# Optimization experiments

Measured on AMD Instinct MI355X. Metric: run time of the kernel, lower is better.

## Reference

```python
import jax, jax.numpy as jnp
import numpy as np

N_NODES = 100000
N_EDGES = 1600000
IN_F = 128
OUT_F = 128
EDGE_F = 16


def setup_inputs() -> dict:
    key = jax.random.key(0)
    ks = jax.random.split(key, 8)
    H = jax.random.normal(ks[0], (N_NODES, IN_F), dtype=jnp.float32)
    edge_index = jax.random.randint(ks[1], (2, N_EDGES), 0, N_ODES_ := N_NODES, dtype=jnp.int64) if False else jax.random.randint(ks[1], (2, N_EDGES), 0, N_NODES, dtype=jnp.int32).astype(jnp.int64)
    edge_attr = jax.random.normal(ks[2], (N_EDGES, EDGE_F), dtype=jnp.float32)
    We = jax.random.normal(ks[3], (EDGE_F, IN_F), dtype=jnp.float32) * (1.0 / np.sqrt(EDGE_F))
    be = jnp.zeros((IN_F,), dtype=jnp.float32)
    W1 = jax.random.normal(ks[4], (IN_F, OUT_F), dtype=jnp.float32) * (1.0 / np.sqrt(IN_F))
    b1 = jnp.zeros((OUT_F,), dtype=jnp.float32)
    W2 = jax.random.normal(ks[5], (OUT_F, OUT_F), dtype=jnp.float32) * (1.0 / np.sqrt(OUT_F))
    b2 = jnp.zeros((OUT_F,), dtype=jnp.float32)
    return {"H": H, "edge_index": edge_index, "edge_attr": edge_attr,
            "We": We, "be": be, "W1": W1, "b1": b1, "W2": W2, "b2": b2}


def reference(H, edge_index, edge_attr, We, be, W1, b1, W2, b2):
    # edge_mlp: Linear(edge_attr_dim -> in_features)
    edge_messages = edge_attr @ We + be                       # [E, in_f]
    # gather by src, add edge messages
    messages = H[edge_index[0]] + edge_messages               # [E, in_f]
    # scatter_add by dst with dim_size = N
    aggregated = jax.ops.segment_sum(messages, edge_index[1], num_segments=H.shape[0])  # [N, in_f]
    # node_mlp: Linear -> ReLU -> Linear
    h = jax.nn.relu(aggregated @ W1 + b1)                     # [N, out_f]
    out = h @ W2 + b2                                         # [N, out_f]
    return out
```

## Files before the change

kernel.cpp:

```cpp
#include <hip/hip_runtime.h>

#define IN_F 128
#define EF 16

typedef short bf16x8 __attribute__((ext_vector_type(8)));
typedef float f32x4  __attribute__((ext_vector_type(4)));

__device__ __forceinline__ unsigned short f2b(float f) {
    unsigned b = __float_as_uint(f);
    b += 0x7fffu + ((b >> 16) & 1u);
    return (unsigned short)(b >> 16);
}
__device__ __forceinline__ float blo(unsigned u) { return __uint_as_float(u << 16); }
__device__ __forceinline__ float bhi(unsigned u) { return __uint_as_float(u & 0xffff0000u); }


__global__ __launch_bounds__(256) void pre_kernel(
    const float* __restrict__ H, unsigned short* __restrict__ Hb, int n4,
    const int* __restrict__ ei, int* __restrict__ counts,
    int* __restrict__ rank, int E,
    const float* __restrict__ W1, unsigned short* __restrict__ W1t,
    const float* __restrict__ W2, unsigned short* __restrict__ W2t,
    int h2b_blocks, int hist_blocks)
{
    int b = blockIdx.x;
    if (b < h2b_blocks) {
        int i = b * 256 + threadIdx.x;
        if (i < n4) {
            float4 v = ((const float4*)H)[i];
            ushort4 r;
            r.x = f2b(v.x); r.y = f2b(v.y); r.z = f2b(v.z); r.w = f2b(v.w);
            ((ushort4*)Hb)[i] = r;
        }
    } else if (b < h2b_blocks + hist_blocks) {
        int e = (b - h2b_blocks) * 256 + threadIdx.x;
        if (e < E) rank[e] = atomicAdd(&counts[ei[E + e]], 1);
    } else {
        int idx = (b - h2b_blocks - hist_blocks) * 256 + threadIdx.x;
        int w = idx >> 14;
        int r = idx & 16383;
        int n = r >> 7, k = r & 127;
        if (w == 0) W1t[n * IN_F + k] = f2b(W1[k * IN_F + n]);
        else        W2t[n * IN_F + k] = f2b(W2[k * IN_F + n]);
    }
}

__global__ __launch_bounds__(256) void hist_kernel(
    const int* __restrict__ ei, int* __restrict__ counts,
    int* __restrict__ rank, int E)
{
    int e = blockIdx.x * 256 + threadIdx.x;
    if (e >= E) return;
    rank[e] = atomicAdd(&counts[ei[E + e]], 1);
}

__global__ __launch_bounds__(256) void scan_blocks_kernel(
    const int* __restrict__ in, int* __restrict__ out,
    int* __restrict__ partials, int n)
{
    __shared__ int sdata[256];
    const int t = threadIdx.x;
    const int idx0 = blockIdx.x * 1024 + t * 4;
    int v[4];
    #pragma unroll
    for (int i = 0; i < 4; i++) { int idx = idx0 + i; v[i] = (idx < n) ? in[idx] : 0; }
    int s = v[0] + v[1] + v[2] + v[3];
    sdata[t] = s;
    __syncthreads();
    for (int off = 1; off < 256; off <<= 1) {
        int x = (t >= off) ? sdata[t - off] : 0;
        __syncthreads();
        sdata[t] += x;
        __syncthreads();
    }
    if (t == 255) partials[blockIdx.x] = sdata[255];
    int run = (t > 0) ? sdata[t - 1] : 0;
    #pragma unroll
    for (int i = 0; i < 4; i++) {
        int idx = idx0 + i;
        if (idx < n) out[idx] = run;
        run += v[i];
    }
}

__global__ __launch_bounds__(256) void scan_add_fused_kernel(
    int* __restrict__ out, const int* __restrict__ partials, int n)
{
    __shared__ int sw[4];
    const int t = threadIdx.x;
    const int g = blockIdx.x >> 2;
    int v = 0;
    for (int j = t; j < g; j += 256) v += partials[j];
    #pragma unroll
    for (int off = 1; off < 64; off <<= 1) v += __shfl_xor(v, off, 64);
    if ((t & 63) == 0) sw[t >> 6] = v;
    __syncthreads();
    int P = sw[0] + sw[1] + sw[2] + sw[3];
    int idx = blockIdx.x * 256 + t;
    if (idx < n) out[idx] += P;
}

__global__ __launch_bounds__(256) void build_kernel(
    const int* __restrict__ ei, int2* __restrict__ sorted,
    const int* __restrict__ offsets, const int* __restrict__ rank, int E)
{
    int e = blockIdx.x * 256 + threadIdx.x;
    if (e >= E) return;
    int src = ei[e];
    int dst = ei[E + e];
    int pos = offsets[dst] + rank[e];
    sorted[pos] = make_int2(src, e);
}

__global__ __launch_bounds__(256) void ea_reduce_kernel(
    const float* __restrict__ EA,
    const int2* __restrict__ sorted,
    const int* __restrict__ offsets,
    float* __restrict__ aggE,
    int N)
{
    int n = blockIdx.x * 4 + (threadIdx.x >> 6);
    if (n >= N) return;
    int lane = threadIdx.x & 63;
    int sub  = lane >> 4;
    int f    = lane & 15;
    int s = offsets[n];
    int e_end = offsets[n + 1];
    float acc = 0.f;
    int i = s + sub;
    for (; i + 4 < e_end; i += 8) {
        int e0 = sorted[i].y;
        int e1 = sorted[i + 4].y;
        float v0 = EA[(long long)e0 * EF + f];
        float v1 = EA[(long long)e1 * EF + f];
        acc += v0 + v1;
    }
    for (; i < e_end; i += 4) {
        int e0 = sorted[i].y;
        acc += EA[(long long)e0 * EF + f];
    }
    acc += __shfl_xor(acc, 16, 64);
    acc += __shfl_xor(acc, 32, 64);
    if (sub == 0) aggE[n * EF + f] = acc;
}

__global__ __launch_bounds__(256) void gather_agg_kernel(
    const unsigned short* __restrict__ Hb,
    const int2* __restrict__ sorted,
    const int* __restrict__ offsets,
    const float* __restrict__ aggE,
    const float* __restrict__ We,
    const float* __restrict__ be,
    unsigned short* __restrict__ Ab,
    int N)
{
    int n = blockIdx.x * 4 + (threadIdx.x >> 6);
    if (n >= N) return;
    int lane = threadIdx.x & 63;
    int half = lane >> 5;
    int l32  = lane & 31;
    int s = offsets[n];
    int e_end = offsets[n + 1];
    float a0 = 0.f, a1 = 0.f, a2 = 0.f, a3 = 0.f;
    int i = s + half;
    for (; i + 6 < e_end; i += 8) {
        int s0 = sorted[i].x;
        int s1 = sorted[i + 2].x;
        int s2 = sorted[i + 4].x;
        int s3 = sorted[i + 6].x;
        uint2 u0 = *(const uint2*)(Hb + (long long)s0 * IN_F + l32 * 4);
        uint2 u1 = *(const uint2*)(Hb + (long long)s1 * IN_F + l32 * 4);
        uint2 u2 = *(const uint2*)(Hb + (long long)s2 * IN_F + l32 * 4);
        uint2 u3 = *(const uint2*)(Hb + (long long)s3 * IN_F + l32 * 4);
        a0 += (blo(u0.x) + blo(u1.x)) + (blo(u2.x) + blo(u3.x));
        a1 += (bhi(u0.x) + bhi(u1.x)) + (bhi(u2.x) + bhi(u3.x));
        a2 += (blo(u0.y) + blo(u1.y)) + (blo(u2.y) + blo(u3.y));
        a3 += (bhi(u0.y) + bhi(u1.y)) + (bhi(u2.y) + bhi(u3.y));
    }
    for (; i < e_end; i += 2) {
        int se = sorted[i].x;
        uint2 u = *(const uint2*)(Hb + (long long)se * IN_F + l32 * 4);
        a0 += blo(u.x); a1 += bhi(u.x); a2 += blo(u.y); a3 += bhi(u.y);
    }
    a0 += __shfl_xor(a0, 32, 64);
    a1 += __shfl_xor(a1, 32, 64);
    a2 += __shfl_xor(a2, 32, 64);
    a3 += __shfl_xor(a3, 32, 64);

    const int c4 = l32 * 4;
    const float deg = (float)(e_end - s);
    float4 bev = *(const float4*)&be[c4];
    float vx = a0 + deg * bev.x;
    float vy = a1 + deg * bev.y;
    float vz = a2 + deg * bev.z;
    float vw = a3 + deg * bev.w;
    #pragma unroll
    for (int k = 0; k < EF; k++) {
        float ak = aggE[n * EF + k];
        float4 w = *(const float4*)&We[k * IN_F + c4];
        vx += ak * w.x; vy += ak * w.y; vz += ak * w.z; vw += ak * w.w;
    }
    if (half == 0) {
        ushort4 o;
        o.x = f2b(vx); o.y = f2b(vy); o.z = f2b(vz); o.w = f2b(vw);
        *(ushort4*)&Ab[(long long)n * IN_F + c4] = o;
    }
}

__global__ __launch_bounds__(256) void gather_f32_kernel(
    const float* __restrict__ H,
    const float* __restrict__ EA,
    const int2* __restrict__ sorted,
    const int* __restrict__ offsets,
    float* __restrict__ agg,
    float* __restrict__ aggE,
    float* __restrict__ degf,
    int N)
{
    int n = blockIdx.x * 4 + (threadIdx.x >> 6);
    if (n >= N) return;
    int lane = threadIdx.x & 63;
    int half = lane >> 5;
    int l32  = lane & 31;
    int s = offsets[n];
    int e_end = offsets[n + 1];
    float4 acc = make_float4(0.f, 0.f, 0.f, 0.f);
    float accE = 0.f;
    int i = s + half;
    for (; i + 6 < e_end; i += 8) {
        int2 s0 = sorted[i];
        int2 s1 = sorted[i + 2];
        int2 s2 = sorted[i + 4];
        int2 s3 = sorted[i + 6];
        float4 v0 = *(const float4*)(H + (long long)s0.x * IN_F + l32 * 4);
        float4 v1 = *(const float4*)(H + (long long)s1.x * IN_F + l32 * 4);
        float4 v2 = *(const float4*)(H + (long long)s2.x * IN_F + l32 * 4);
        float4 v3 = *(const float4*)(H + (long long)s3.x * IN_F + l32 * 4);
        float e0 = 0.f, e1 = 0.f, e2 = 0.f, e3 = 0.f;
        if (l32 < EF) {
            e0 = EA[(long long)s0.y * EF + l32];
            e1 = EA[(long long)s1.y * EF + l32];
            e2 = EA[(long long)s2.y * EF + l32];
            e3 = EA[(long long)s3.y * EF + l32];
        }
        acc.x += (v0.x + v1.x) + (v2.x + v3.x);
        acc.y += (v0.y + v1.y) + (v2.y + v3.y);
        acc.z += (v0.z + v1.z) + (v2.z + v3.z);
        acc.w += (v0.w + v1.w) + (v2.w + v3.w);
        accE  += (e0 + e1) + (e2 + e3);
    }
    for (; i < e_end; i += 2) {
        int2 se = sorted[i];
        float4 v = *(const float4*)(H + (long long)se.x * IN_F + l32 * 4);
        acc.x += v.x; acc.y += v.y; acc.z += v.z; acc.w += v.w;
        if (l32 < EF) accE += EA[(long long)se.y * EF + l32];
    }
    acc.x += __shfl_xor(acc.x, 32, 64);
    acc.y += __shfl_xor(acc.y, 32, 64);
    acc.z += __shfl_xor(acc.z, 32, 64);
    acc.w += __shfl_xor(acc.w, 32, 64);
    accE  += __shfl_xor(accE, 32, 64);
    if (half == 0) {
        *(float4*)(agg + (long long)n * IN_F + l32 * 4) = acc;
        if (l32 < EF) aggE[n * EF + l32] = accE;
        if (l32 == 0) degf[n] = (float)(e_end - s);
    }
}

__global__ __launch_bounds__(256) void edge_scatter_kernel(
    const float* __restrict__ H,
    const int* __restrict__ ei,
    const float* __restrict__ EA,
    float* __restrict__ agg,
    float* __restrict__ aggE,
    float* __restrict__ deg,
    int E)
{
    long long gid = (long long)blockIdx.x * 256 + threadIdx.x;
    int e = (int)(gid >> 7);
    if (e >= E) return;
    int f = (int)(gid & 127);
    int src = ei[e];
    int dst = ei[E + e];
    float m = H[(long long)src * IN_F + f];
    atomicAdd(&agg[(long long)dst * IN_F + f], m);
    if (f < EF) atomicAdd(&aggE[dst * EF + f], EA[e * EF + f]);
    if (f == 0) atomicAdd(&deg[dst], 1.0f);
}


#define XPITCH 136
__global__ __launch_bounds__(256) void mlp_mfma_kernel(
    const unsigned short* __restrict__ Ab,
    const unsigned short* __restrict__ W1t,
    const unsigned short* __restrict__ W2t,
    const float* __restrict__ b1, const float* __restrict__ b2,
    float* __restrict__ out, int N)
{
    __shared__ unsigned short sW[128 * XPITCH];
    __shared__ unsigned short sX[64 * XPITCH];
    const int t    = threadIdx.x;
    const int tile = blockIdx.x * 64;
    const int lane = t & 63;
    const int wv   = t >> 6;
    const int quad = lane >> 4;
    const int lr   = lane & 15;
    const int M0   = wv * 16;

    {
        const uint4 z = make_uint4(0, 0, 0, 0);
        #pragma unroll
        for (int j = 0; j < 4; j++) {
            int idx = t + 256 * j;
            int row = idx >> 4, c = idx & 15;
            uint4 v = z;
            if (tile + row < N) v = ((const uint4*)Ab)[(long long)(tile + row) * 16 + c];
            ((uint4*)sX)[row * 17 + c] = v;
        }
        #pragma unroll
        for (int j = 0; j < 8; j++) {
            int idx = t + 256 * j;
            int row = idx >> 4, c = idx & 15;
            ((uint4*)sW)[row * 17 + c] = ((const uint4*)W1t)[idx];
        }
    }
    __syncthreads();

    f32x4 acc[8];
    bf16x8 af[4];
    const f32x4 zero = {0.f, 0.f, 0.f, 0.f};

    #pragma unroll
    for (int kt = 0; kt < 4; kt++)
        af[kt] = *(const bf16x8*)&sX[(M0 + lr) * XPITCH + kt * 32 + quad * 8];
    #pragma unroll
    for (int nt = 0; nt < 8; nt++) {
        acc[nt] = zero;
        #pragma unroll
        for (int kt = 0; kt < 4; kt++) {
            bf16x8 bf = *(const bf16x8*)&sW[(nt * 16 + lr) * XPITCH + kt * 32 + quad * 8];
            acc[nt] = __builtin_amdgcn_mfma_f32_16x16x32_bf16(af[kt], bf, acc[nt], 0, 0, 0);
        }
    }
    #pragma unroll
    for (int nt = 0; nt < 8; nt++) {
        int col = nt * 16 + lr;
        float bias = b1[col];
        #pragma unroll
        for (int r = 0; r < 4; r++) {
            float v = fmaxf(acc[nt][r] + bias, 0.f);
            sX[(M0 + quad * 4 + r) * XPITCH + col] = f2b(v);
        }
    }
    __syncthreads();
    #pragma unroll
    for (int j = 0; j < 8; j++) {
        int idx = t + 256 * j;
        int row = idx >> 4, c = idx & 15;
        ((uint4*)sW)[row * 17 + c] = ((const uint4*)W2t)[idx];
    }
    __syncthreads();

    #pragma unroll
    for (int kt = 0; kt < 4; kt++)
        af[kt] = *(const bf16x8*)&sX[(M0 + lr) * XPITCH + kt * 32 + quad * 8];
    #pragma unroll
    for (int nt = 0; nt < 8; nt++) {
        acc[nt] = zero;
        #pragma unroll
        for (int kt = 0; kt < 4; kt++) {
            bf16x8 bf = *(const bf16x8*)&sW[(nt * 16 + lr) * XPITCH + kt * 32 + quad * 8];
            acc[nt] = __builtin_amdgcn_mfma_f32_16x16x32_bf16(af[kt], bf, acc[nt], 0, 0, 0);
        }
    }
    #pragma unroll
    for (int nt = 0; nt < 8; nt++) {
        int col = nt * 16 + lr;
        float bias = b2[col];
        #pragma unroll
        for (int r = 0; r < 4; r++) {
            int row = tile + M0 + quad * 4 + r;
            if (row < N) out[(long long)row * IN_F + col] = acc[nt][r] + bias;
        }
    }
}

__global__ __launch_bounds__(256) void node_mlp_kernel(
    float* agg_out,
    const float* __restrict__ aggE,
    const float* __restrict__ degf,
    const float* __restrict__ We, const float* __restrict__ be,
    const float* __restrict__ W1, const float* __restrict__ b1,
    const float* __restrict__ W2, const float* __restrict__ b2,
    int N)
{
    __shared__ float sA[32][IN_F];
    __shared__ float sH[32][IN_F];
    const int t  = threadIdx.x;
    const int c4 = (t & 31) * 4;
    const int r0 = t >> 5;

    const int tile = blockIdx.x * 32;
    if (tile >= N) return;
    int rows = N - tile;
    if (rows > 32) rows = 32;

    {
        const float4 bev = *(const float4*)&be[c4];
        #pragma unroll
        for (int i = 0; i < 4; i++) {
            int rr = r0 + 8 * i;
            float4 v = make_float4(0.f, 0.f, 0.f, 0.f);
            if (rr < rows) {
                long long r = tile + rr;
                v = *(const float4*)&agg_out[r * IN_F + c4];
                float d = degf[r];
                v.x += d * bev.x; v.y += d * bev.y; v.z += d * bev.z; v.w += d * bev.w;
                #pragma unroll
                for (int k = 0; k < EF; k++) {
                    float a = aggE[r * EF + k];
                    float4 w = *(const float4*)&We[k * IN_F + c4];
                    v.x += a * w.x; v.y += a * w.y; v.z += a * w.z; v.w += a * w.w;
                }
            }
            *(float4*)&sA[rr][c4] = v;
        }
    }
    __syncthreads();
    {
        const float4 bv = *(const float4*)&b1[c4];
        float4 a0 = bv, a1 = bv, a2 = bv, a3 = bv;
        for (int k = 0; k < IN_F; k++) {
            float4 w = *(const float4*)&W1[k * IN_F + c4];
            float x0 = sA[r0][k], x1 = sA[r0 + 8][k], x2 = sA[r0 + 16][k], x3 = sA[r0 + 24][k];
            a0.x += x0 * w.x; a0.y += x0 * w.y; a0.z += x0 * w.z; a0.w += x0 * w.w;
            a1.x += x1 * w.x; a1.y += x1 * w.y; a1.z += x1 * w.z; a1.w += x1 * w.w;
            a2.x += x2 * w.x; a2.y += x2 * w.y; a2.z += x2 * w.z; a2.w += x2 * w.w;
            a3.x += x3 * w.x; a3.y += x3 * w.y; a3.z += x3 * w.z; a3.w += x3 * w.w;
        }
        a0.x = fmaxf(a0.x, 0.f); a0.y = fmaxf(a0.y, 0.f); a0.z = fmaxf(a0.z, 0.f); a0.w = fmaxf(a0.w, 0.f);
        a1.x = fmaxf(a1.x, 0.f); a1.y = fmaxf(a1.y, 0.f); a1.z = fmaxf(a1.z, 0.f); a1.w = fmaxf(a1.w, 0.f);
        a2.x = fmaxf(a2.x, 0.f); a2.y = fmaxf(a2.y, 0.f); a2.z = fmaxf(a2.z, 0.f); a2.w = fmaxf(a2.w, 0.f);
        a3.x = fmaxf(a3.x, 0.f); a3.y = fmaxf(a3.y, 0.f); a3.z = fmaxf(a3.z, 0.f); a3.w = fmaxf(a3.w, 0.f);
        *(float4*)&sH[r0][c4]      = a0;
        *(float4*)&sH[r0 + 8][c4]  = a1;
        *(float4*)&sH[r0 + 16][c4] = a2;
        *(float4*)&sH[r0 + 24][c4] = a3;
    }
    __syncthreads();
    {
        const float4 bv = *(const float4*)&b2[c4];
        float4 a0 = bv, a1 = bv, a2 = bv, a3 = bv;
        for (int k = 0; k < IN_F; k++) {
            float4 w = *(const float4*)&W2[k * IN_F + c4];
            float x0 = sH[r0][k], x1 = sH[r0 + 8][k], x2 = sH[r0 + 16][k], x3 = sH[r0 + 24][k];
            a0.x += x0 * w.x; a0.y += x0 * w.y; a0.z += x0 * w.z; a0.w += x0 * w.w;
            a1.x += x1 * w.x; a1.y += x1 * w.y; a1.z += x1 * w.z; a1.w += x1 * w.w;
            a2.x += x2 * w.x; a2.y += x2 * w.y; a2.z += x2 * w.z; a2.w += x2 * w.w;
            a3.x += x3 * w.x; a3.y += x3 * w.y; a3.z += x3 * w.z; a3.w += x3 * w.w;
        }
        #pragma unroll
        for (int i = 0; i < 4; i++) {
            int rr = r0 + 8 * i;
            if (rr < rows) {
                float4 v = (i == 0) ? a0 : (i == 1) ? a1 : (i == 2) ? a2 : a3;
                *(float4*)&agg_out[(long long)(tile + rr) * IN_F + c4] = v;
            }
        }
    }
}

extern "C" void kernel_launch(void* const* d_in, const int* in_sizes, int n_in,
                              void* d_out, int out_size, void* d_ws, size_t ws_size,
                              hipStream_t stream) {
    const float* H  = (const float*)d_in[0];
    const int*   ei = (const int*)d_in[1];
    const float* EA = (const float*)d_in[2];
    const float* We = (const float*)d_in[3];
    const float* be = (const float*)d_in[4];
    const float* W1 = (const float*)d_in[5];
    const float* b1 = (const float*)d_in[6];
    const float* W2 = (const float*)d_in[7];
    const float* b2 = (const float*)d_in[8];
    float* out = (float*)d_out;

    const int N = in_sizes[0] / IN_F;
    const int E = in_sizes[2] / EF;

    char* p = (char*)d_ws;
    auto alloc = [&](size_t bytes) { char* r = p; p += (bytes + 255) & ~(size_t)255; return r; };
    int2*  sorted   = (int2*)alloc((size_t)E * sizeof(int2));
    int*   rank     = (int*)alloc((size_t)E * sizeof(int));
    float* degf     = (float*)alloc((size_t)N * sizeof(float));
    float* aggE     = (float*)alloc((size_t)N * EF * sizeof(float));
    int*   counts   = (int*)alloc((size_t)(N + 1) * sizeof(int));
    int*   offsets  = (int*)alloc((size_t)(N + 1) * sizeof(int));
    int*   partials = (int*)alloc(1024 * sizeof(int));
    size_t need_base = (size_t)(p - (char*)d_ws);
    unsigned short* Hb = (unsigned short*)alloc((size_t)N * IN_F * sizeof(unsigned short));
    unsigned short* Ab  = (unsigned short*)alloc((size_t)N * IN_F * sizeof(unsigned short));
    unsigned short* W1t = (unsigned short*)alloc((size_t)IN_F * IN_F * sizeof(unsigned short));
    unsigned short* W2t = (unsigned short*)alloc((size_t)IN_F * IN_F * sizeof(unsigned short));
    size_t need_mfma = (size_t)(p - (char*)d_ws);

    const int n_scan = N + 1;
    const int B = (n_scan + 1023) / 1024;

    if (ws_size >= need_mfma && B <= 1024) {
        hipMemsetAsync(counts, 0, (size_t)(N + 1) * sizeof(int), stream);
        const int n4 = N * IN_F / 4;
        const int h2b_blocks  = (n4 + 255) / 256;
        const int hist_blocks = (E + 255) / 256;
        pre_kernel<<<h2b_blocks + hist_blocks + 128, 256, 0, stream>>>(
            H, Hb, n4, ei, counts, rank, E, W1, W1t, W2, W2t, h2b_blocks, hist_blocks);
        scan_blocks_kernel<<<B, 256, 0, stream>>>(counts, offsets, partials, n_scan);
        scan_add_fused_kernel<<<(n_scan + 255) / 256, 256, 0, stream>>>(offsets, partials, n_scan);
        build_kernel<<<(E + 255) / 256, 256, 0, stream>>>(ei, sorted, offsets, rank, E);
        ea_reduce_kernel<<<(N + 3) / 4, 256, 0, stream>>>(EA, sorted, offsets, aggE, N);
        gather_agg_kernel<<<(N + 3) / 4, 256, 0, stream>>>(
            Hb, sorted, offsets, aggE, We, be, Ab, N);
        mlp_mfma_kernel<<<(N + 63) / 64, 256, 0, stream>>>(Ab, W1t, W2t, b1, b2, out, N);
    } else if (ws_size >= need_base && B <= 1024) {
        hipMemsetAsync(counts, 0, (size_t)(N + 1) * sizeof(int), stream);
        hist_kernel<<<(E + 255) / 256, 256, 0, stream>>>(ei, counts, rank, E);
        scan_blocks_kernel<<<B, 256, 0, stream>>>(counts, offsets, partials, n_scan);
        scan_add_fused_kernel<<<(n_scan + 255) / 256, 256, 0, stream>>>(offsets, partials, n_scan);
        build_kernel<<<(E + 255) / 256, 256, 0, stream>>>(ei, sorted, offsets, rank, E);
        gather_f32_kernel<<<(N + 3) / 4, 256, 0, stream>>>(H, EA, sorted, offsets, out, aggE, degf, N);
        node_mlp_kernel<<<(N + 31) / 32, 256, 0, stream>>>(out, aggE, degf, We, be, W1, b1, W2, b2, N);
    } else {
        float* f_aggE = (float*)d_ws;
        float* f_deg  = f_aggE + (size_t)N * EF;
        hipMemsetAsync(d_out, 0, (size_t)N * IN_F * sizeof(float), stream);
        hipMemsetAsync(d_ws, 0, (size_t)N * (EF + 1) * sizeof(float), stream);
        long long tot = (long long)E * IN_F;
        edge_scatter_kernel<<<(int)((tot + 255) / 256), 256, 0, stream>>>(H, ei, EA, out, f_aggE, f_deg, E);
        node_mlp_kernel<<<(N + 31) / 32, 256, 0, stream>>>(out, f_aggE, f_deg, We, be, W1, b1, W2, b2, N);
    }
}
```

Baseline: 491.8 us.

## Fold edge-MLP into W1 and merge edge-attr and feature gathers into one kernel

Precomputes We@W1 and be@W1 in the prep kernel so the edge-attribute contribution is added directly in the first MLP layer's accumulator init, rather than being expanded to 128 features before bf16 conversion. The separate edge-attr reduction and H gather kernels are merged into one launch, with alternating blocks doing each task, so they can run concurrently and the dependency between them is gone. Ab now holds only the gathered H sum, and the MLP kernel reads aggE and degree per row. This adds per-thread FMAs and register pressure in the MFMA kernel, and changes the rounding slightly.

```diff
diff --git a/kernel.cpp b/kernel.cpp
--- a/kernel.cpp
+++ b/kernel.cpp
@@ -21,6 +21,8 @@
     int* __restrict__ rank, int E,
     const float* __restrict__ W1, unsigned short* __restrict__ W1t,
     const float* __restrict__ W2, unsigned short* __restrict__ W2t,
+    const float* __restrict__ We, const float* __restrict__ be,
+    float* __restrict__ Wea, float* __restrict__ bea,
     int h2b_blocks, int hist_blocks)
 {
     int b = blockIdx.x;
@@ -35,13 +37,26 @@
     } else if (b < h2b_blocks + hist_blocks) {
         int e = (b - h2b_blocks) * 256 + threadIdx.x;
         if (e < E) rank[e] = atomicAdd(&counts[ei[E + e]], 1);
-    } else {
+    } else if (b < h2b_blocks + hist_blocks + 128) {
         int idx = (b - h2b_blocks - hist_blocks) * 256 + threadIdx.x;
         int w = idx >> 14;
         int r = idx & 16383;
         int n = r >> 7, k = r & 127;
         if (w == 0) W1t[n * IN_F + k] = f2b(W1[k * IN_F + n]);
         else        W2t[n * IN_F + k] = f2b(W2[k * IN_F + n]);
+    } else {
+        int idx = (b - h2b_blocks - hist_blocks - 128) * 256 + threadIdx.x;
+        if (idx < EF * IN_F) {
+            int k = idx >> 7, n = idx & 127;
+            float acc = 0.f;
+            for (int j = 0; j < IN_F; j++) acc += We[k * IN_F + j] * W1[j * IN_F + n];
+            Wea[k * IN_F + n] = acc;
+        } else if (idx < EF * IN_F + IN_F) {
+            int n = idx - EF * IN_F;
+            float acc = 0.f;
+            for (int j = 0; j < IN_F; j++) acc += be[j] * W1[j * IN_F + n];
+            bea[n] = acc;
+        }
     }
 }
 
@@ -112,98 +127,75 @@
     sorted[pos] = make_int2(src, e);
 }
 
-__global__ __launch_bounds__(256) void ea_reduce_kernel(
+__global__ __launch_bounds__(256) void gather_ea_kernel(
+    const unsigned short* __restrict__ Hb,
     const float* __restrict__ EA,
     const int2* __restrict__ sorted,
     const int* __restrict__ offsets,
+    unsigned short* __restrict__ Ab,
     float* __restrict__ aggE,
     int N)
 {
-    int n = blockIdx.x * 4 + (threadIdx.x >> 6);
+    const int bt = blockIdx.x & 1;
+    const int bg = blockIdx.x >> 1;
+    int n = bg * 4 + (threadIdx.x >> 6);
     if (n >= N) return;
     int lane = threadIdx.x & 63;
-    int sub  = lane >> 4;
-    int f    = lane & 15;
     int s = offsets[n];
     int e_end = offsets[n + 1];
-    float acc = 0.f;
-    int i = s + sub;
-    for (; i + 4 < e_end; i += 8) {
-        int e0 = sorted[i].y;
-        int e1 = sorted[i + 4].y;
-        float v0 = EA[(long long)e0 * EF + f];
-        float v1 = EA[(long long)e1 * EF + f];
-        acc += v0 + v1;
-    }
-    for (; i < e_end; i += 4) {
-        int e0 = sorted[i].y;
-        acc += EA[(long long)e0 * EF + f];
-    }
-    acc += __shfl_xor(acc, 16, 64);
-    acc += __shfl_xor(acc, 32, 64);
-    if (sub == 0) aggE[n * EF + f] = acc;
-}
-
-__global__ __launch_bounds__(256) void gather_agg_kernel(
-    const unsigned short* __restrict__ Hb,
-    const int2* __restrict__ sorted,
-    const int* __restrict__ offsets,
-    const float* __restrict__ aggE,
-    const float* __restrict__ We,
-    const float* __restrict__ be,
-    unsigned short* __restrict__ Ab,
-    int N)
-{
-    int n = blockIdx.x * 4 + (threadIdx.x >> 6);
-    if (n >= N) return;
-    int lane = threadIdx.x & 63;
-    int half = lane >> 5;
-    int l32  = lane & 31;
-    int s = offsets[n];
-    int e_end = offsets[n + 1];
-    float a0 = 0.f, a1 = 0.f, a2 = 0.f, a3 = 0.f;
-    int i = s + half;
-    for (; i + 6 < e_end; i += 8) {
-        int s0 = sorted[i].x;
-        int s1 = sorted[i + 2].x;
-        int s2 = sorted[i + 4].x;
-        int s3 = sorted[i + 6].x;
-        uint2 u0 = *(const uint2*)(Hb + (long long)s0 * IN_F + l32 * 4);
-        uint2 u1 = *(const uint2*)(Hb + (long long)s1 * IN_F + l32 * 4);
-        uint2 u2 = *(const uint2*)(Hb + (long long)s2 * IN_F + l32 * 4);
-        uint2 u3 = *(const uint2*)(Hb + (long long)s3 * IN_F + l32 * 4);
-        a0 += (blo(u0.x) + blo(u1.x)) + (blo(u2.x) + blo(u3.x));
-        a1 += (bhi(u0.x) + bhi(u1.x)) + (bhi(u2.x) + bhi(u3.x));
-        a2 += (blo(u0.y) + blo(u1.y)) + (blo(u2.y) + blo(u3.y));
-        a3 += (bhi(u0.y) + bhi(u1.y)) + (bhi(u2.y) + bhi(u3.y));
-    }
-    for (; i < e_end; i += 2) {
-        int se = sorted[i].x;
-        uint2 u = *(const uint2*)(Hb + (long long)se * IN_F + l32 * 4);
-        a0 += blo(u.x); a1 += bhi(u.x); a2 += blo(u.y); a3 += bhi(u.y);
-    }
-    a0 += __shfl_xor(a0, 32, 64);
-    a1 += __shfl_xor(a1, 32, 64);
-    a2 += __shfl_xor(a2, 32, 64);
-    a3 += __shfl_xor(a3, 32, 64);
-
-    const int c4 = l32 * 4;
-    const float deg = (float)(e_end - s);
-    float4 bev = *(const float4*)&be[c4];
-    float vx = a0 + deg * bev.x;
-    float vy = a1 + deg * bev.y;
-    float vz = a2 + deg * bev.z;
-    float vw = a3 + deg * bev.w;
-    #pragma unroll
-    for (int k = 0; k < EF; k++) {
-        float ak = aggE[n * EF + k];
-        float4 w = *(const float4*)&We[k * IN_F + c4];
-        vx += ak * w.x; vy += ak * w.y; vz += ak * w.z; vw += ak * w.w;
-    }
-    if (half == 0) {
-        ushort4 o;
-        o.x = f2b(vx); o.y = f2b(vy); o.z = f2b(vz); o.w = f2b(vw);
-        *(ushort4*)&Ab[(long long)n * IN_F + c4] = o;
+
+    if (bt == 0) {
+        int half = lane >> 5;
+        int l32  = lane & 31;
+        float a0 = 0.f, a1 = 0.f, a2 = 0.f, a3 = 0.f;
+        int i = s + half;
+        for (; i + 6 < e_end; i += 8) {
+            int s0 = sorted[i].x;
+            int s1 = sorted[i + 2].x;
+            int s2 = sorted[i + 4].x;
+            int s3 = sorted[i + 6].x;
+            uint2 u0 = *(const uint2*)(Hb + (long long)s0 * IN_F + l32 * 4);
+            uint2 u1 = *(const uint2*)(Hb + (long long)s1 * IN_F + l32 * 4);
+            uint2 u2 = *(const uint2*)(Hb + (long long)s2 * IN_F + l32 * 4);
+            uint2 u3 = *(const uint2*)(Hb + (long long)s3 * IN_F + l32 * 4);
+            a0 += (blo(u0.x) + blo(u1.x)) + (blo(u2.x) + blo(u3.x));
+            a1 += (bhi(u0.x) + bhi(u1.x)) + (bhi(u2.x) + bhi(u3.x));
+            a2 += (blo(u0.y) + blo(u1.y)) + (blo(u2.y) + blo(u3.y));
+            a3 += (bhi(u0.y) + bhi(u1.y)) + (bhi(u2.y) + bhi(u3.y));
+        }
+        for (; i < e_end; i += 2) {
+            int se = sorted[i].x;
+            uint2 u = *(const uint2*)(Hb + (long long)se * IN_F + l32 * 4);
+            a0 += blo(u.x); a1 += bhi(u.x); a2 += blo(u.y); a3 += bhi(u.y);
+        }
+        a0 += __shfl_xor(a0, 32, 64);
+        a1 += __shfl_xor(a1, 32, 64);
+        a2 += __shfl_xor(a2, 32, 64);
+        a3 += __shfl_xor(a3, 32, 64);
+        if (half == 0) {
+            ushort4 o;
+            o.x = f2b(a0); o.y = f2b(a1); o.z = f2b(a2); o.w = f2b(a3);
+            *(ushort4*)&Ab[(long long)n * IN_F + l32 * 4] = o;
+        }
+    } else {
+        int sub = lane >> 4;
+        int f   = lane & 15;
+        float acc = 0.f;
+        int i = s + sub;
+        for (; i + 4 < e_end; i += 8) {
+            int e0 = sorted[i].y;
+            int e1 = sorted[i + 4].y;
+            float v0 = EA[(long long)e0 * EF + f];
+            float v1 = EA[(long long)e1 * EF + f];
+            acc += v0 + v1;
+        }
+        for (; i < e_end; i += 4) {
+            int e0 = sorted[i].y;
+            acc += EA[(long long)e0 * EF + f];
+        }
+        acc += __shfl_xor(acc, 16, 64);
+        acc += __shfl_xor(acc, 32, 64);
+        if (sub == 0) aggE[n * EF + f] = acc;
     }
 }
 
@@ -294,6 +286,10 @@
     const unsigned short* __restrict__ Ab,
     const unsigned short* __restrict__ W1t,
     const unsigned short* __restrict__ W2t,
+    const float* __restrict__ aggE,
+    const int* __restrict__ offsets,
+    const float* __restrict__ Wea,
+    const float* __restrict__ bea,
     const float* __restrict__ b1, const float* __restrict__ b2,
     float* __restrict__ out, int N)
 {
@@ -324,18 +320,49 @@
             ((uint4*)sW)[row * 17 + c] = ((const uint4*)W1t)[idx];
         }
     }
+
+    float degv[4];
+    f32x4 aeq[4][4];
+    #pragma unroll
+    for (int r = 0; r < 4; r++) {
+        int row = tile + M0 + quad * 4 + r;
+        if (row < N) {
+            degv[r] = (float)(offsets[row + 1] - offsets[row]);
+            #pragma unroll
+            for (int q = 0; q < 4; q++)
+                aeq[r][q] = *(const f32x4*)&aggE[(long long)row * EF + q * 4];
+        } else {
+            degv[r] = 0.f;
+            #pragma unroll
+            for (int q = 0; q < 4; q++) aeq[r][q] = (f32x4){0.f, 0.f, 0.f, 0.f};
+        }
+    }
     __syncthreads();
 
     f32x4 acc[8];
     bf16x8 af[4];
-    const f32x4 zero = {0.f, 0.f, 0.f, 0.f};
 
     #pragma unroll
     for (int kt = 0; kt < 4; kt++)
         af[kt] = *(const bf16x8*)&sX[(M0 + lr) * XPITCH + kt * 32 + quad * 8];
     #pragma unroll
     for (int nt = 0; nt < 8; nt++) {
-        acc[nt] = zero;
+        int col = nt * 16 + lr;
+        float base = b1[col];
+        float beac = bea[col];
+        float c0 = base + degv[0] * beac;
+        float c1 = base + degv[1] * beac;
+        float c2 = base + degv[2] * beac;
+        float c3 = base + degv[3] * beac;
+        #pragma unroll
+        for (int k = 0; k < EF; k++) {
+            float wk = Wea[k * IN_F + col];
+            c0 += ((const float*)&aeq[0][k >> 2])[k & 3] * wk;
+            c1 += ((const float*)&aeq[1][k >> 2])[k & 3] * wk;
+            c2 += ((const float*)&aeq[2][k >> 2])[k & 3] * wk;
+            c3 += ((const float*)&aeq[3][k >> 2])[k & 3] * wk;
+        }
+        acc[nt] = (f32x4){c0, c1, c2, c3};
         #pragma unroll
         for (int kt = 0; kt < 4; kt++) {
             bf16x8 bf = *(const bf16x8*)&sW[(nt * 16 + lr) * XPITCH + kt * 32 + quad * 8];
@@ -345,10 +372,9 @@
     #pragma unroll
     for (int nt = 0; nt < 8; nt++) {
         int col = nt * 16 + lr;
-        float bias = b1[col];
         #pragma unroll
         for (int r = 0; r < 4; r++) {
-            float v = fmaxf(acc[nt][r] + bias, 0.f);
+            float v = fmaxf(acc[nt][r], 0.f);
             sX[(M0 + quad * 4 + r) * XPITCH + col] = f2b(v);
         }
     }
@@ -361,6 +387,7 @@
     }
     __syncthreads();
 
+    const f32x4 zero = {0.f, 0.f, 0.f, 0.f};
     #pragma unroll
     for (int kt = 0; kt < 4; kt++)
         af[kt] = *(const bf16x8*)&sX[(M0 + lr) * XPITCH + kt * 32 + quad * 8];
@@ -501,6 +528,8 @@
     unsigned short* Ab  = (unsigned short*)alloc((size_t)N * IN_F * sizeof(unsigned short));
     unsigned short* W1t = (unsigned short*)alloc((size_t)IN_F * IN_F * sizeof(unsigned short));
     unsigned short* W2t = (unsigned short*)alloc((size_t)IN_F * IN_F * sizeof(unsigned short));
+    float* Wea = (float*)alloc((size_t)EF * IN_F * sizeof(float));
+    float* bea = (float*)alloc((size_t)IN_F * sizeof(float));
     size_t need_mfma = (size_t)(p - (char*)d_ws);
 
     const int n_scan = N + 1;
@@ -511,15 +540,17 @@
         const int n4 = N * IN_F / 4;
         const int h2b_blocks  = (n4 + 255) / 256;
         const int hist_blocks = (E + 255) / 256;
-        pre_kernel<<<h2b_blocks + hist_blocks + 128, 256, 0, stream>>>(
-            H, Hb, n4, ei, counts, rank, E, W1, W1t, W2, W2t, h2b_blocks, hist_blocks);
+        const int wea_blocks  = (EF * IN_F + IN_F + 255) / 256;
+        pre_kernel<<<h2b_blocks + hist_blocks + 128 + wea_blocks, 256, 0, stream>>>(
+            H, Hb, n4, ei, counts, rank, E, W1, W1t, W2, W2t, We, be, Wea, bea,
+            h2b_blocks, hist_blocks);
         scan_blocks_kernel<<<B, 256, 0, stream>>>(counts, offsets, partials, n_scan);
         scan_add_fused_kernel<<<(n_scan + 255) / 256, 256, 0, stream>>>(offsets, partials, n_scan);
         build_kernel<<<(E + 255) / 256, 256, 0, stream>>>(ei, sorted, offsets, rank, E);
-        ea_reduce_kernel<<<(N + 3) / 4, 256, 0, stream>>>(EA, sorted, offsets, aggE, N);
-        gather_agg_kernel<<<(N + 3) / 4, 256, 0, stream>>>(
-            Hb, sorted, offsets, aggE, We, be, Ab, N);
-        mlp_mfma_kernel<<<(N + 63) / 64, 256, 0, stream>>>(Ab, W1t, W2t, b1, b2, out, N);
+        gather_ea_kernel<<<2 * ((N + 3) / 4), 256, 0, stream>>>(
+            Hb, EA, sorted, offsets, Ab, aggE, N);
+        mlp_mfma_kernel<<<(N + 63) / 64, 256, 0, stream>>>(
+            Ab, W1t, W2t, aggE, offsets, Wea, bea, b1, b2, out, N);
     } else if (ws_size >= need_base && B <= 1024) {
         hipMemsetAsync(counts, 0, (size_t)(N + 1) * sizeof(int), stream);
         hist_kernel<<<(E + 255) / 256, 256, 0, stream>>>(ei, counts, rank, E);
```

New measurement: 487.2 us. Within noise of the previous version (-0.9%).
